# Performance work log

Measured on AMD Instinct MI355X. Metric: run time of the kernel, lower is better.

## Reference

```python
import jax, jax.numpy as jnp
import numpy as np

PAD, BOS, EOS, UNK = 0, 1, 2, 3
B, S, V, D, L = 256, 512, 50000, 256, 128

def setup_inputs() -> dict:
    key = jax.random.key(0)
    ks = jax.random.split(key, 12)
    vocab_tensor = jax.random.randint(ks[0], (B, S), 4, V)
    parent_idx = jax.random.randint(ks[1], (B, S), 0, S)
    pbond = jax.random.randint(ks[2], (B, S), 0, 4)
    bond = jax.random.randint(ks[3], (B, S), 0, 4)
    patom = jax.random.randint(ks[4], (B, S), 0, 16)
    atom = jax.random.randint(ks[5], (B, S), 0, 16)
    btype = jax.random.randint(ks[6], (B, S), 0, 4)
    order_tensor = jnp.stack([parent_idx, pbond, bond, patom, atom, btype], axis=-1)
    lengths = jax.random.randint(ks[7], (B,), 1, S + 1)
    mask_tensor = jnp.arange(S)[None, :] < lengths[:, None]  # ragged prefix masks
    eps = jax.random.normal(ks[8], (B, L), dtype=jnp.float32)
    sc = 1.0 / np.sqrt(D)
    emb = jax.random.normal(ks[9], (V, D), dtype=jnp.float32) * sc
    Wm = jax.random.normal(ks[10], (D, L), dtype=jnp.float32) * sc
    Wv = jax.random.normal(ks[11], (D, L), dtype=jnp.float32) * sc
    Wlin = jax.random.normal(jax.random.fold_in(key, 20), (L, D), dtype=jnp.float32) / np.sqrt(L)
    Wout = jax.random.normal(jax.random.fold_in(key, 21), (D, D), dtype=jnp.float32) * sc
    return {
        'vocab_tensor': vocab_tensor, 'order_tensor': order_tensor, 'mask_tensor': mask_tensor,
        'eps': eps, 'emb': emb, 'Wm': Wm, 'bm': jnp.zeros((L,), jnp.float32),
        'Wv': Wv, 'bv': jnp.zeros((L,), jnp.float32), 'Wlin': Wlin,
        'blin': jnp.zeros((D,), jnp.float32), 'Wout': Wout, 'bout': jnp.zeros((D,), jnp.float32),
    }

def _forward(vocab_tensor, order_tensor, mask_tensor, eps, emb, Wm, bm, Wv, bv, Wlin, blin, Wout, bout):
    # --- mask bond-pos columns (torch.where assignments, vectorized) ---
    # (columns 1 and 2 set to -1 where masked; kept implicitly via vt/pad handling)
    # --- calc_chem_z path: masked vocab, parent gather, edge one-hot ---
    vt = jnp.where(mask_tensor, vocab_tensor, PAD)                      # [B,S]
    vocab_emb = emb[vt]                                                 # [B,S,D]
    oi = order_tensor[..., 0]
    oi = jnp.where(oi == -1, BOS, oi)
    parent = jnp.where(mask_tensor, jnp.take_along_axis(vt, oi, axis=1), PAD)
    parent = parent.at[:, 0].set(BOS)
    parent_emb = emb[parent]                                            # [B,S,D]
    idx = jnp.clip(order_tensor[..., 5] - 1, -1, None)
    edge_type = jnp.where((idx >= 0)[..., None],
                          jax.nn.one_hot(jnp.clip(idx, 0), 3, dtype=jnp.float32), 0.0)  # [B,S,3]
    # pooling stand-in for (undefined) StructureEncoder -> [B,D]
    m = mask_tensor[..., None].astype(jnp.float32)
    enc = ((vocab_emb + parent_emb) * m).sum(1) / jnp.maximum(m.sum(1), 1.0)
    enc = enc * (1.0 + 0.0 * edge_type.sum())  # keep edge_type in graph
    # --- LatentSampler ---
    mean = enc @ Wm + bm
    log_var = enc @ Wv + bv
    z = mean + eps * jnp.exp(0.5 * log_var)
    memory = z @ Wlin + blin                                            # [B,D]
    # --- vectorized bos/eos/pad sequence assembly (the hot loop in torch) ---
    inp = jnp.concatenate([jnp.full((B, 1), BOS, vocab_tensor.dtype), vocab_tensor], axis=1)  # [B,S+1]
    mask_ex = jnp.concatenate([jnp.ones((B, 1), bool), mask_tensor], axis=1)
    tgt = jnp.roll(inp, -1, axis=1)
    first_false = jnp.argmax(~mask_ex, axis=1)                          # first eos position
    has_false = jnp.any(~mask_ex, axis=1)
    pos = jnp.arange(S + 1)[None, :]
    tgt = jnp.where(has_false[:, None] & (pos == first_false[:, None] - 1), EOS, tgt)
    kill = has_false[:, None] & (pos >= first_false[:, None])
    tgt = jnp.where(kill, PAD, tgt)
    inp = jnp.where(kill, PAD, inp)
    # edge_index assembly (faithful, consumed by decoder in original)
    padneg = jnp.full((B, 1), -1, order_tensor.dtype)
    edge_index = jnp.concatenate([padneg, jnp.where(mask_tensor, order_tensor[..., 0], -2) + 1], axis=1)
    # --- embedding lookups + decoder stand-in + output head ---
    node_embed = emb[inp]                                               # [B,S+1,D]
    dec = node_embed + memory[:, None, :]
    dec = dec + 0.0 * edge_index[..., None].astype(jnp.float32)         # keep edge_index in graph
    word_emb = dec @ Wout + bout
    tgt_emb = emb[tgt]
    valid = (tgt != PAD)
    sq = (word_emb - tgt_emb) ** 2 * valid[..., None]
    token_loss = sq.sum() / jnp.maximum(valid.sum() * D, 1).astype(jnp.float32)
    kl = -0.5 * jnp.sum(1.0 + log_var - mean ** 2 - jnp.exp(log_var)) / B
    return token_loss, kl

def reference(vocab_tensor, order_tensor, mask_tensor, eps, emb, Wm, bm, Wv, bv, Wlin, blin, Wout, bout):
    return _forward(vocab_tensor, order_tensor, mask_tensor, eps, emb, Wm, bm, Wv, bv, Wlin, blin, Wout, bout)
```

## Files before the change

kernel.cpp:

```cpp
#include <hip/hip_runtime.h>

#define B_ 256
#define S_ 512
#define V_ 50000
#define D_ 256
#define L_ 128
#define NGB 512
#define NENC 256
#define NCH (V_ / 16)
#define NSPLIT 8
#define K2B (B_ * NSPLIT)

typedef __attribute__((ext_vector_type(8))) short short8;
typedef __attribute__((ext_vector_type(4))) float floatx4;

#define OFF_SQP 16
#define OFF_KL  (OFF_SQP + K2B)
#define OFF_CNT (OFF_KL + 256)
#define OFF_Q   (OFF_CNT + 256)
#define OFF_P   (OFF_Q + B_ * D_)
#define OFF_EB  (OFF_P + V_ * D_ / 2)

__device__ __forceinline__ unsigned short f2bf(float x) {
    unsigned u = __float_as_uint(x);
    u += 0x7FFFu + ((u >> 16) & 1u);
    return (unsigned short)(u >> 16);
}
__device__ __forceinline__ float bf2f(unsigned short u) {
    return __uint_as_float(((unsigned)u) << 16);
}

__global__ __launch_bounds__(256, 2) void fused1(
    const int* __restrict__ vocab, const int* __restrict__ order,
    const int* __restrict__ mask, const float* __restrict__ emb,
    const float* __restrict__ eps, const float* __restrict__ Wm,
    const float* __restrict__ bm, const float* __restrict__ Wv,
    const float* __restrict__ bv, const float* __restrict__ Wlin,
    const float* __restrict__ blin, const float* __restrict__ Wout,
    const float* __restrict__ bout, float* __restrict__ ws) {
    __shared__ __align__(16) char smem[16384];
    const int tid = threadIdx.x;

    if (blockIdx.x < NGB) {
        unsigned short* __restrict__ P = (unsigned short*)(ws + OFF_P);
        unsigned short* __restrict__ EB = (unsigned short*)(ws + OFF_EB);
        const int lane = tid & 63, wv = tid >> 6;
        const int lo = lane & 15, hi = lane >> 4;
        short8 bfr[4][8];
#pragma unroll
        for (int nt = 0; nt < 4; ++nt)
#pragma unroll
            for (int kk = 0; kk < 8; ++kk) {
                const float* wp = Wout + (size_t)(hi * 8 + kk * 32) * D_ +
                                  wv * 64 + nt * 16 + lo;
                short8 w;
#pragma unroll
                for (int e = 0; e < 8; ++e) w[e] = (short)f2bf(wp[(size_t)e * D_]);
                bfr[nt][kk] = w;
            }
        int ch = blockIdx.x;
        float4 R[4];
        {
            const float4* src = (const float4*)emb + (size_t)ch * 1024;
#pragma unroll
            for (int i = 0; i < 4; ++i) R[i] = src[i * 256 + tid];
        }
        for (; ch < NCH; ch += NGB) {
#pragma unroll
            for (int i = 0; i < 4; ++i) {
                const int e = (i * 256 + tid) * 4;
                const int row = e >> 8, colb = (e & 255) * 2;
                const int byt = (row * 512 + colb) ^ ((row & 7) << 4);
                ushort4 h;
                h.x = f2bf(R[i].x); h.y = f2bf(R[i].y);
                h.z = f2bf(R[i].z); h.w = f2bf(R[i].w);
                *(ushort4*)(smem + byt) = h;
            }
            __syncthreads();
            const int chn = ch + NGB;
            float4 Rn[4] = {R[0], R[1], R[2], R[3]};
            if (chn < NCH) {
                const float4* src = (const float4*)emb + (size_t)chn * 1024;
#pragma unroll
                for (int i = 0; i < 4; ++i) Rn[i] = src[i * 256 + tid];
            }
            floatx4 acc[4];
#pragma unroll
            for (int nt = 0; nt < 4; ++nt) acc[nt] = (floatx4){0.f, 0.f, 0.f, 0.f};
#pragma unroll
            for (int kk = 0; kk < 8; ++kk) {
                const int byt = (lo * 512 + hi * 16 + kk * 64) ^ ((lo & 7) << 4);
                short8 a = *(const short8*)(smem + byt);
#pragma unroll
                for (int nt = 0; nt < 4; ++nt)
                    acc[nt] = __builtin_amdgcn_mfma_f32_16x16x32_bf16(
                        a, bfr[nt][kk], acc[nt], 0, 0, 0);
            }
            {
                const int o0 = tid * 32;
                const int sw = ((o0 >> 9) & 7) << 4;
                ushort4 e0 = *(const ushort4*)(smem + (o0 ^ sw));
                ushort4 e1 = *(const ushort4*)(smem + ((o0 + 16) ^ sw));
                ushort4* dst = (ushort4*)((char*)EB + (size_t)ch * 8192 + o0);
                dst[0] = e0; dst[1] = e1;
            }
#pragma unroll
            for (int r = 0; r < 4; ++r) {
                const int row = hi * 4 + r;
#pragma unroll
                for (int nt = 0; nt < 4; ++nt) {
                    const int col = wv * 64 + nt * 16 + lo;
                    *(unsigned short*)(smem + 8192 + row * 512 + col * 2) =
                        f2bf(acc[nt][r]);
                }
            }
            __syncthreads();
            {
                const int o0 = tid * 32;
                ushort4 c0 = *(const ushort4*)(smem + 8192 + o0);
                ushort4 c1 = *(const ushort4*)(smem + 8192 + o0 + 16);
                ushort4* dst = (ushort4*)((char*)P + (size_t)ch * 8192 + o0);
                dst[0] = c0; dst[1] = c1;
            }
#pragma unroll
            for (int i = 0; i < 4; ++i) R[i] = Rn[i];
        }
        return;
    }
    int* s_id1 = (int*)smem;
    int* s_id2 = s_id1 + S_;
    float4* s_part = (float4*)(smem + 4096);
    float* s_enc = (float*)(smem + 7168);
    float* s_mean = (float*)(smem + 8192);
    float* s_lv = (float*)(smem + 8704);
    float* s_z = (float*)(smem + 9216);
    float* s_mem = (float*)(smem + 9728);
    float* s_red = (float*)(smem + 10752);
    int* s_cntp = (int*)(smem + 11776);
    const int b = blockIdx.x - NGB;
    if (tid == 0) *s_cntp = 0;
    __syncthreads();
    for (int j = tid; j < S_; j += 256) {
        const int mk = mask[b * S_ + j];
        int id1 = 0, id2 = 0;
        if (mk) {
            id1 = vocab[b * S_ + j];
            if (j == 0) {
                id2 = 1;
            } else {
                int oi = order[(size_t)(b * S_ + j) * 6];
                if (oi == -1) oi = 1;
                id2 = mask[b * S_ + oi] ? vocab[b * S_ + oi] : 0;
            }
        }
        s_id1[j] = id1;
        s_id2[j] = id2;
        unsigned long long bal = __ballot(mk != 0);
        if ((tid & 63) == 0) atomicAdd(s_cntp, __popcll(bal));
    }
    __syncthreads();
    const int cnt = *s_cntp;
    const int jg = tid >> 6, d4 = tid & 63;
    const float4* eb4 = (const float4*)emb;
    float4 a = {0.f, 0.f, 0.f, 0.f};
#pragma unroll 4
    for (int j = jg; j < cnt; j += 4) {
        float4 x = eb4[(size_t)s_id1[j] * 64 + d4];
        float4 y = eb4[(size_t)s_id2[j] * 64 + d4];
        a.x += x.x + y.x; a.y += x.y + y.y;
        a.z += x.z + y.z; a.w += x.w + y.w;
    }
    if (jg) s_part[(jg - 1) * 64 + d4] = a;
    __syncthreads();
    if (jg == 0) {
#pragma unroll
        for (int g = 0; g < 3; ++g) {
            float4 p = s_part[g * 64 + d4];
            a.x += p.x; a.y += p.y; a.z += p.z; a.w += p.w;
        }
        const float inv = 1.f / fmaxf((float)cnt, 1.f);
        a.x *= inv; a.y *= inv; a.z *= inv; a.w *= inv;
        ((float4*)s_enc)[d4] = a;
    }
    __syncthreads();
    {
        const int l = tid & (L_ - 1);
        const float* W = (tid < L_) ? Wm : Wv;
        const float* bb = (tid < L_) ? bm : bv;
        float dot = bb[l];
        for (int d = 0; d < D_; ++d) dot = fmaf(s_enc[d], W[d * L_ + l], dot);
        if (tid < L_) s_mean[l] = dot; else s_lv[l] = dot;
    }
    __syncthreads();
    float klp = 0.f;
    if (tid < L_) {
        float mn = s_mean[tid], lv = s_lv[tid];
        s_z[tid] = mn + eps[b * L_ + tid] * expf(0.5f * lv);
        klp = 1.f + lv - mn * mn - expf(lv);
    }
    s_red[tid] = klp;
    __syncthreads();
    for (int s = 128; s > 0; s >>= 1) {
        if (tid < s) s_red[tid] += s_red[tid + s];
        __syncthreads();
    }
    if (tid == 0) {
        ws[OFF_KL + b] = s_red[0];
        ((int*)ws)[OFF_CNT + b] = cnt;
    }
    {
        float mem = blin[tid];
        for (int l2 = 0; l2 < L_; ++l2) mem = fmaf(s_z[l2], Wlin[l2 * D_ + tid], mem);
        s_mem[tid] = mem;
    }
    __syncthreads();
    {
        float qv = bout[tid];
        for (int k = 0; k < D_; ++k) qv = fmaf(s_mem[k], Wout[k * D_ + tid], qv);
        ws[OFF_Q + b * D_ + tid] = qv;
    }
}

__global__ __launch_bounds__(256) void scan2(const int* __restrict__ vocab,
                                             float* __restrict__ ws) {
    __shared__ int s_sid[80];
    __shared__ float s_wred[4];
    const int tid = threadIdx.x;
    const int b = blockIdx.x >> 3, part = blockIdx.x & 7;
    const unsigned short* __restrict__ P = (const unsigned short*)(ws + OFF_P);
    const unsigned short* __restrict__ EB = (const unsigned short*)(ws + OFF_EB);
    const int cnt = ((const int*)ws)[OFF_CNT + b];
    const int npos = cnt + 1;
    const int per = (npos + NSPLIT - 1) / NSPLIT;
    const int j0 = part * per;
    const int jend = min(j0 + per, npos);
    const int lo_s = (j0 > 0) ? j0 - 1 : 0;
    const int nstage = min(jend, cnt) - lo_s;
    if (tid < nstage) s_sid[tid] = vocab[b * S_ + lo_s + tid];
    __syncthreads();
    const int jgq = tid >> 6, lane = tid & 63, c = lane * 4;
    const float4 q4 = *(const float4*)(ws + OFF_Q + b * D_ + c);
    float acc = 0.f;
    for (int jj = j0 + jgq * 4; jj < jend; jj += 16) {
        int inp[4], tgt[4];
        float wgt[4];
#pragma unroll
        for (int u = 0; u < 4; ++u) {
            const int j = jj + u;
            const bool v = (j < jend);
            const int jc = v ? j : jj;
            inp[u] = (jc == 0) ? 1 : s_sid[jc - 1 - lo_s];
            tgt[u] = (jc < cnt) ? s_sid[jc - lo_s] : ((cnt < S_) ? 2 : 1);
            wgt[u] = v ? 1.f : 0.f;
        }
        ushort4 pv[4], tv[4];
#pragma unroll
        for (int u = 0; u < 4; ++u) {
            pv[u] = *(const ushort4*)(P + (size_t)inp[u] * D_ + c);
            tv[u] = *(const ushort4*)(EB + (size_t)tgt[u] * D_ + c);
        }
#pragma unroll
        for (int u = 0; u < 4; ++u) {
            float d0 = bf2f(pv[u].x) + q4.x - bf2f(tv[u].x);
            float d1 = bf2f(pv[u].y) + q4.y - bf2f(tv[u].y);
            float d2 = bf2f(pv[u].z) + q4.z - bf2f(tv[u].z);
            float d3 = bf2f(pv[u].w) + q4.w - bf2f(tv[u].w);
            float s = fmaf(d0, d0, fmaf(d1, d1, fmaf(d2, d2, d3 * d3)));
            acc = fmaf(wgt[u], s, acc);
        }
    }
#pragma unroll
    for (int off = 32; off; off >>= 1) acc += __shfl_down(acc, off, 64);
    if (lane == 0) s_wred[jgq] = acc;
    __syncthreads();
    if (tid == 0)
        ws[OFF_SQP + blockIdx.x] = s_wred[0] + s_wred[1] + s_wred[2] + s_wred[3];
}

__global__ __launch_bounds__(256) void finalize3(const float* __restrict__ ws,
                                                 float* __restrict__ out) {
    __shared__ float s_red[256];
    const int tid = threadIdx.x;
    float sq = 0.f;
#pragma unroll
    for (int i = 0; i < NSPLIT; ++i) sq += ws[OFF_SQP + i * 256 + tid];
    s_red[tid] = sq;
    __syncthreads();
    for (int s = 128; s > 0; s >>= 1) {
        if (tid < s) s_red[tid] += s_red[tid + s];
        __syncthreads();
    }
    const float sq_tot = s_red[0];
    __syncthreads();
    s_red[tid] = ws[OFF_KL + tid];
    __syncthreads();
    for (int s = 128; s > 0; s >>= 1) {
        if (tid < s) s_red[tid] += s_red[tid + s];
        __syncthreads();
    }
    const float kl_tot = s_red[0];
    __syncthreads();
    s_red[tid] = (float)(((const int*)ws)[OFF_CNT + tid] + 1);
    __syncthreads();
    for (int s = 128; s > 0; s >>= 1) {
        if (tid < s) s_red[tid] += s_red[tid + s];
        __syncthreads();
    }
    if (tid == 0) {
        float denom = s_red[0] * (float)D_;
        if (denom < 1.f) denom = 1.f;
        out[0] = sq_tot / denom;
        out[1] = -0.5f * kl_tot / (float)B_;
    }
}

extern "C" void kernel_launch(void* const* d_in, const int* in_sizes, int n_in,
                              void* d_out, int out_size, void* d_ws, size_t ws_size,
                              hipStream_t stream) {
    const int* vocab = (const int*)d_in[0];
    const int* order = (const int*)d_in[1];
    const int* mask  = (const int*)d_in[2];
    const float* eps  = (const float*)d_in[3];
    const float* emb  = (const float*)d_in[4];
    const float* Wm   = (const float*)d_in[5];
    const float* bm   = (const float*)d_in[6];
    const float* Wv   = (const float*)d_in[7];
    const float* bv   = (const float*)d_in[8];
    const float* Wlin = (const float*)d_in[9];
    const float* blin = (const float*)d_in[10];
    const float* Wout = (const float*)d_in[11];
    const float* bout = (const float*)d_in[12];

    float* ws = (float*)d_ws;
    fused1<<<NGB + NENC, 256, 0, stream>>>(vocab, order, mask, emb, eps, Wm, bm,
                                           Wv, bv, Wlin, blin, Wout, bout, ws);
    scan2<<<K2B, 256, 0, stream>>>(vocab, ws);
    finalize3<<<1, 256, 0, stream>>>(ws, (float*)d_out);
}
```

Before: 172.2 us.

## Pre-pack Wout to bf16 fragments, swizzle LDS staging, raise GEMM block count

Result: no change. 171.1 us (-0.7%).

```diff
diff --git a/kernel.cpp b/kernel.cpp
--- a/kernel.cpp
+++ b/kernel.cpp
@@ -5,7 +5,7 @@
 #define V_ 50000
 #define D_ 256
 #define L_ 128
-#define NGB 512
+#define NGB 768
 #define NENC 256
 #define NCH (V_ / 16)
 #define NSPLIT 8
@@ -20,6 +20,7 @@
 #define OFF_Q   (OFF_CNT + 256)
 #define OFF_P   (OFF_Q + B_ * D_)
 #define OFF_EB  (OFF_P + V_ * D_ / 2)
+#define OFF_WB  (OFF_EB + V_ * D_ / 2)
 
 __device__ __forceinline__ unsigned short f2bf(float x) {
     unsigned u = __float_as_uint(x);
@@ -28,6 +29,24 @@
 }
 __device__ __forceinline__ float bf2f(unsigned short u) {
     return __uint_as_float(((unsigned)u) << 16);
+}
+
+__global__ __launch_bounds__(256) void prep0(const float* __restrict__ Wout,
+                                             float* __restrict__ ws) {
+    unsigned short* __restrict__ Wb = (unsigned short*)(ws + OFF_WB);
+    const int t = blockIdx.x * 256 + threadIdx.x;
+    const int idx0 = t * 4;
+    const int kk = idx0 >> 13;
+    const int col = (idx0 >> 5) & 255;
+    const int hi = (idx0 >> 3) & 3;
+    const int e0 = idx0 & 7;
+    const int kbase = kk * 32 + hi * 8 + e0;
+    ushort4 h;
+    h.x = f2bf(Wout[(size_t)(kbase + 0) * D_ + col]);
+    h.y = f2bf(Wout[(size_t)(kbase + 1) * D_ + col]);
+    h.z = f2bf(Wout[(size_t)(kbase + 2) * D_ + col]);
+    h.w = f2bf(Wout[(size_t)(kbase + 3) * D_ + col]);
+    ((ushort4*)Wb)[t] = h;
 }
 
 __global__ __launch_bounds__(256, 2) void fused1(
@@ -44,20 +63,16 @@
     if (blockIdx.x < NGB) {
         unsigned short* __restrict__ P = (unsigned short*)(ws + OFF_P);
         unsigned short* __restrict__ EB = (unsigned short*)(ws + OFF_EB);
+        const unsigned short* __restrict__ Wb = (const unsigned short*)(ws + OFF_WB);
         const int lane = tid & 63, wv = tid >> 6;
         const int lo = lane & 15, hi = lane >> 4;
         short8 bfr[4][8];
 #pragma unroll
         for (int nt = 0; nt < 4; ++nt)
 #pragma unroll
-            for (int kk = 0; kk < 8; ++kk) {
-                const float* wp = Wout + (size_t)(hi * 8 + kk * 32) * D_ +
-                                  wv * 64 + nt * 16 + lo;
-                short8 w;
-#pragma unroll
-                for (int e = 0; e < 8; ++e) w[e] = (short)f2bf(wp[(size_t)e * D_]);
-                bfr[nt][kk] = w;
-            }
+            for (int kk = 0; kk < 8; ++kk)
+                bfr[nt][kk] = *(const short8*)(Wb + kk * 8192 +
+                                               (wv * 64 + nt * 16 + lo) * 32 + hi * 8);
         int ch = blockIdx.x;
         float4 R[4];
         {
@@ -110,15 +125,16 @@
 #pragma unroll
                 for (int nt = 0; nt < 4; ++nt) {
                     const int col = wv * 64 + nt * 16 + lo;
-                    *(unsigned short*)(smem + 8192 + row * 512 + col * 2) =
-                        f2bf(acc[nt][r]);
+                    const int off = (row * 512 + col * 2) ^ (((row >> 2) & 3) << 5);
+                    *(unsigned short*)(smem + 8192 + off) = f2bf(acc[nt][r]);
                 }
             }
             __syncthreads();
             {
                 const int o0 = tid * 32;
-                ushort4 c0 = *(const ushort4*)(smem + 8192 + o0);
-                ushort4 c1 = *(const ushort4*)(smem + 8192 + o0 + 16);
+                const int sw = (((o0 >> 9) >> 2) & 3) << 5;
+                ushort4 c0 = *(const ushort4*)(smem + 8192 + (o0 ^ sw));
+                ushort4 c1 = *(const ushort4*)(smem + 8192 + ((o0 + 16) ^ sw));
                 ushort4* dst = (ushort4*)((char*)P + (size_t)ch * 8192 + o0);
                 dst[0] = c0; dst[1] = c1;
             }
@@ -332,6 +348,7 @@
     const float* bout = (const float*)d_in[12];
 
     float* ws = (float*)d_ws;
+    prep0<<<64, 256, 0, stream>>>(Wout, ws);
     fused1<<<NGB + NENC, 256, 0, stream>>>(vocab, order, mask, emb, eps, Wm, bm,
                                            Wv, bv, Wlin, blin, Wout, bout, ws);
     scan2<<<K2B, 256, 0, stream>>>(vocab, ws);
```
